# Kernel optimization log

Measured on AMD Instinct MI355X. Metric: run time of the kernel, lower is better.

The kernel has to match this reference:

```python
import jax, jax.numpy as jnp
import numpy as np

PI = 3.1415926  # matches the truncated pi used in the torch source
BS = 8          # DCT block size (qmat.shape[1:] == (8, 8))
NQ = 16         # number of learned quant matrices (qmat.shape[0])
IMG = 64        # nn.Fold output_size=(64, 64)


def dct_matrix(n):
    # Reproduces the (slightly nonstandard) basis built in DCT2d.__init__.
    C = np.zeros((n, n), dtype=np.float32)
    C[0, :] = np.sqrt(1.0 / n)
    for i in range(1, n):
        for j in range(n):
            C[i, j] = np.cos(PI * i * (2 * j + 1) / (2.0 * n)) * np.sqrt(2.0 / n)
    return jnp.asarray(C)


def setup_inputs() -> dict:
    key = jax.random.key(0)
    ks = jax.random.split(key, 9)
    B, Ch = 32, 256
    x = jax.random.normal(ks[0], (B, Ch, IMG, IMG), dtype=jnp.float32)
    noise_level = jax.random.uniform(ks[1], (1,), dtype=jnp.float32)
    # learned parameters
    qmat = jax.random.uniform(ks[2], (NQ, BS, BS), dtype=jnp.float32)
    qmat_weights = jnp.ones((NQ,), dtype=jnp.float32)
    # noise_level_net: Linear(1,16) -> GELU -> Linear(16,16) -> GELU -> Linear(16, 2+NQ)
    w1 = jax.random.normal(ks[3], (1, 16), dtype=jnp.float32) * 0.5
    b1 = jnp.zeros((16,), dtype=jnp.float32)
    w2 = jax.random.normal(ks[4], (16, 16), dtype=jnp.float32) * 0.25
    b2 = jnp.zeros((16,), dtype=jnp.float32)
    w3 = jax.random.normal(ks[5], (16, 2 + NQ), dtype=jnp.float32) * 0.25
    b3 = jnp.zeros((2 + NQ,), dtype=jnp.float32)
    return {"x": x, "noise_level": noise_level, "qmat": qmat,
            "qmat_weights": qmat_weights, "w1": w1, "b1": b1,
            "w2": w2, "b2": b2, "w3": w3, "b3": b3}


def reference(x, noise_level, qmat, qmat_weights, w1, b1, w2, b2, w3, b3):
    B, Ch, H, W = x.shape
    Cm = dct_matrix(BS)
    Cmt = Cm.T

    # noise_level_net (torch.nn.GELU default = exact erf)
    h = jax.nn.gelu(noise_level @ w1 + b1, approximate=False)
    h = jax.nn.gelu(h @ w2 + b2, approximate=False)
    nr = h @ w3 + b3  # [2 + NQ]

    qw = jax.nn.softmax(qmat_weights) * nr[0] + nr[1]          # [NQ]
    learned_qmat = jnp.einsum('i,ihw->hw', qw * nr[2:], qmat)  # [8, 8]

    # unfold into non-overlapping 8x8 blocks: [B*Ch, L, 8, 8], L = (H/8)*(W/8)
    blocks = x.reshape(B * Ch, H // BS, BS, W // BS, BS)
    blocks = blocks.transpose(0, 1, 3, 2, 4).reshape(B * Ch, -1, BS, BS)

    # 2D DCT per block: C @ X @ C^T
    blocks_dct = jnp.einsum('ij,nljk,km->nlim', Cm, blocks, Cmt)
    # IDCT of mask-weighted spectra: C^T @ X @ C
    low = jnp.einsum('ij,nljk,km->nlim', Cmt, blocks_dct * learned_qmat, Cm)
    high = jnp.einsum('ij,nljk,km->nlim', Cmt, blocks_dct * (1.0 - learned_qmat), Cm)

    def fold(b):  # inverse of the unfold above
        b = b.reshape(B * Ch, H // BS, W // BS, BS, BS)
        return b.transpose(0, 1, 3, 2, 4).reshape(B, Ch, H, W)

    return fold(low), fold(high)
```

## Files before the change

### kernel.cpp

```cpp
#include <hip/hip_runtime.h>
#include <math.h>


__host__ __device__ constexpr float cc(int i, int j) {
  constexpr double COS16[32] = {
     1.0,
     0.98078528040323043,
     0.92387953251128674,
     0.83146961230254524,
     0.70710678118654752,
     0.55557023301960222,
     0.38268343236508977,
     0.19509032201612827,
     0.0,
    -0.19509032201612827,
    -0.38268343236508977,
    -0.55557023301960222,
    -0.70710678118654752,
    -0.83146961230254524,
    -0.92387953251128674,
    -0.98078528040323043,
    -1.0,
    -0.98078528040323043,
    -0.92387953251128674,
    -0.83146961230254524,
    -0.70710678118654752,
    -0.55557023301960222,
    -0.38268343236508977,
    -0.19509032201612827,
     0.0,
     0.19509032201612827,
     0.38268343236508977,
     0.55557023301960222,
     0.70710678118654752,
     0.83146961230254524,
     0.92387953251128674,
     0.98078528040323043,
  };
  return (i == 0) ? 0.35355339059327373f
                  : (float)(0.5 * COS16[(i * (2 * j + 1)) % 32]);
}

__global__ void setup_q(const float* __restrict__ noise,
                        const float* __restrict__ qmat,
                        const float* __restrict__ qmw,
                        const float* __restrict__ w1, const float* __restrict__ b1,
                        const float* __restrict__ w2, const float* __restrict__ b2,
                        const float* __restrict__ w3, const float* __restrict__ b3,
                        float* __restrict__ qout) {
  __shared__ double coeff[16];
  if (threadIdx.x == 0) {
    const double inv_sqrt2 = 0.70710678118654752;
    double h1[16], h2[16], nr[18];
    double nl = (double)noise[0];
    for (int j = 0; j < 16; ++j) {
      double v = nl * (double)w1[j] + (double)b1[j];
      h1[j] = 0.5 * v * (1.0 + erf(v * inv_sqrt2));
    }
    for (int j = 0; j < 16; ++j) {
      double v = (double)b2[j];
      for (int i = 0; i < 16; ++i) v += h1[i] * (double)w2[i * 16 + j];
      h2[j] = 0.5 * v * (1.0 + erf(v * inv_sqrt2));
    }
    for (int j = 0; j < 18; ++j) {
      double v = (double)b3[j];
      for (int i = 0; i < 16; ++i) v += h2[i] * (double)w3[i * 18 + j];
      nr[j] = v;
    }
    double mx = (double)qmw[0];
    for (int i = 1; i < 16; ++i) mx = fmax(mx, (double)qmw[i]);
    double e[16], s = 0.0;
    for (int i = 0; i < 16; ++i) { e[i] = exp((double)qmw[i] - mx); s += e[i]; }
    for (int i = 0; i < 16; ++i)
      coeff[i] = (e[i] / s * nr[0] + nr[1]) * nr[2 + i];
  }
  __syncthreads();
  const int t = threadIdx.x;
  double q = 0.0;
  for (int i = 0; i < 16; ++i) q += coeff[i] * (double)qmat[i * 64 + t];
  qout[t] = (float)q;
}

__global__ __launch_bounds__(256) void dct_main(const float* __restrict__ x,
                                                const float* __restrict__ qb,
                                                float* __restrict__ lo,
                                                float* __restrict__ hi) {
  const int gid = blockIdx.x * 256 + threadIdx.x;
  const int base = ((gid >> 6) << 12) | (((gid >> 3) & 7) << 9) | ((gid & 7) << 3);
  const float* px = x + base;

  float X[8][8];
#pragma unroll
  for (int r = 0; r < 8; ++r) {
    const float4 a = *reinterpret_cast<const float4*>(px + r * 64);
    const float4 b = *reinterpret_cast<const float4*>(px + r * 64 + 4);
    X[r][0] = a.x; X[r][1] = a.y; X[r][2] = a.z; X[r][3] = a.w;
    X[r][4] = b.x; X[r][5] = b.y; X[r][6] = b.z; X[r][7] = b.w;
  }

  float U[8][8];
#pragma unroll
  for (int r = 0; r < 8; ++r) {
#pragma unroll
    for (int j = 0; j < 8; ++j) {
      float s = X[r][0] * cc(j, 0);
#pragma unroll
      for (int l = 1; l < 8; ++l) s = fmaf(X[r][l], cc(j, l), s);
      U[r][j] = s;
    }
  }
#pragma unroll
  for (int j = 0; j < 8; ++j) {
    float t[8];
#pragma unroll
    for (int i = 0; i < 8; ++i) {
      float s = cc(i, 0) * U[0][j];
#pragma unroll
      for (int k = 1; k < 8; ++k) s = fmaf(cc(i, k), U[k][j], s);
      t[i] = s;
    }
#pragma unroll
    for (int i = 0; i < 8; ++i) U[i][j] = t[i] * qb[i * 8 + j];
  }
#pragma unroll
  for (int r = 0; r < 8; ++r) {
    float t[8];
#pragma unroll
    for (int j = 0; j < 8; ++j) {
      float s = U[r][0] * cc(0, j);
#pragma unroll
      for (int k = 1; k < 8; ++k) s = fmaf(U[r][k], cc(k, j), s);
      t[j] = s;
    }
#pragma unroll
    for (int j = 0; j < 8; ++j) U[r][j] = t[j];
  }
#pragma unroll
  for (int j = 0; j < 8; ++j) {
    float t[8];
#pragma unroll
    for (int i = 0; i < 8; ++i) {
      float s = cc(0, i) * U[0][j];
#pragma unroll
      for (int k = 1; k < 8; ++k) s = fmaf(cc(k, i), U[k][j], s);
      t[i] = s;
    }
#pragma unroll
    for (int i = 0; i < 8; ++i) U[i][j] = t[i];
  }

  float* plo = lo + base;
  float* phi = hi + base;
#pragma unroll
  for (int r = 0; r < 8; ++r) {
    float4 a = make_float4(U[r][0], U[r][1], U[r][2], U[r][3]);
    float4 b = make_float4(U[r][4], U[r][5], U[r][6], U[r][7]);
    *reinterpret_cast<float4*>(plo + r * 64)     = a;
    *reinterpret_cast<float4*>(plo + r * 64 + 4) = b;
    float4 c = make_float4(X[r][0] - U[r][0], X[r][1] - U[r][1],
                           X[r][2] - U[r][2], X[r][3] - U[r][3]);
    float4 d = make_float4(X[r][4] - U[r][4], X[r][5] - U[r][5],
                           X[r][6] - U[r][6], X[r][7] - U[r][7]);
    *reinterpret_cast<float4*>(phi + r * 64)     = c;
    *reinterpret_cast<float4*>(phi + r * 64 + 4) = d;
  }
}

extern "C" void kernel_launch(void* const* d_in, const int* in_sizes, int n_in,
                              void* d_out, int out_size, void* d_ws, size_t ws_size,
                              hipStream_t stream) {
  const float* x   = (const float*)d_in[0];
  const float* nl  = (const float*)d_in[1];
  const float* qm  = (const float*)d_in[2];
  const float* qmw = (const float*)d_in[3];
  const float* w1  = (const float*)d_in[4];
  const float* b1  = (const float*)d_in[5];
  const float* w2  = (const float*)d_in[6];
  const float* b2  = (const float*)d_in[7];
  const float* w3  = (const float*)d_in[8];
  const float* b3  = (const float*)d_in[9];

  const int n_elem = in_sizes[0];
  float* lo = (float*)d_out;
  float* hi = lo + n_elem;
  float* q  = (float*)d_ws;

  setup_q<<<1, 64, 0, stream>>>(nl, qm, qmw, w1, b1, w2, b2, w3, b3, q);

  const int n_blocks8 = n_elem >> 6;
  const int grid = n_blocks8 >> 8;
  dct_main<<<grid, 256, 0, stream>>>(x, q, lo, hi);
}
```

Before: 466.1 us.

## Fuse quant-matrix setup into DCT kernel and use nontemporal loads/stores

Removes the separate single-block setup kernel and recomputes the small MLP, softmax and 8x8 quant matrix redundantly in every workgroup into shared memory, in float instead of double. Global loads and stores of the streaming image data become nontemporal. This saves one launch and the dependency gap between kernels, at the cost of redundant per-block prologue work, several barriers, and slightly different float precision. Nontemporal hints are meant to reduce cache pollution for the 268 MB-class streaming traffic.

```diff
diff --git a/kernel.cpp b/kernel.cpp
--- a/kernel.cpp
+++ b/kernel.cpp
@@ -1,6 +1,8 @@
 #include <hip/hip_runtime.h>
 #include <math.h>
 
+
+typedef float f4 __attribute__((ext_vector_type(4)));
 
 __host__ __device__ constexpr float cc(int i, int j) {
   constexpr double COS16[32] = {
@@ -41,59 +43,72 @@
                   : (float)(0.5 * COS16[(i * (2 * j + 1)) % 32]);
 }
 
-__global__ void setup_q(const float* __restrict__ noise,
-                        const float* __restrict__ qmat,
-                        const float* __restrict__ qmw,
-                        const float* __restrict__ w1, const float* __restrict__ b1,
-                        const float* __restrict__ w2, const float* __restrict__ b2,
-                        const float* __restrict__ w3, const float* __restrict__ b3,
-                        float* __restrict__ qout) {
-  __shared__ double coeff[16];
-  if (threadIdx.x == 0) {
-    const double inv_sqrt2 = 0.70710678118654752;
-    double h1[16], h2[16], nr[18];
-    double nl = (double)noise[0];
-    for (int j = 0; j < 16; ++j) {
-      double v = nl * (double)w1[j] + (double)b1[j];
-      h1[j] = 0.5 * v * (1.0 + erf(v * inv_sqrt2));
-    }
-    for (int j = 0; j < 16; ++j) {
-      double v = (double)b2[j];
-      for (int i = 0; i < 16; ++i) v += h1[i] * (double)w2[i * 16 + j];
-      h2[j] = 0.5 * v * (1.0 + erf(v * inv_sqrt2));
-    }
-    for (int j = 0; j < 18; ++j) {
-      double v = (double)b3[j];
-      for (int i = 0; i < 16; ++i) v += h2[i] * (double)w3[i * 18 + j];
-      nr[j] = v;
-    }
-    double mx = (double)qmw[0];
-    for (int i = 1; i < 16; ++i) mx = fmax(mx, (double)qmw[i]);
-    double e[16], s = 0.0;
-    for (int i = 0; i < 16; ++i) { e[i] = exp((double)qmw[i] - mx); s += e[i]; }
-    for (int i = 0; i < 16; ++i)
-      coeff[i] = (e[i] / s * nr[0] + nr[1]) * nr[2 + i];
-  }
-  __syncthreads();
-  const int t = threadIdx.x;
-  double q = 0.0;
-  for (int i = 0; i < 16; ++i) q += coeff[i] * (double)qmat[i * 64 + t];
-  qout[t] = (float)q;
-}
-
-__global__ __launch_bounds__(256) void dct_main(const float* __restrict__ x,
-                                                const float* __restrict__ qb,
-                                                float* __restrict__ lo,
-                                                float* __restrict__ hi) {
-  const int gid = blockIdx.x * 256 + threadIdx.x;
+__device__ __forceinline__ float gelu_exact(float v) {
+  return 0.5f * v * (1.0f + erff(v * 0.70710678118654752f));
+}
+
+__global__ __launch_bounds__(256) void dct_fused(
+    const float* __restrict__ x,
+    const float* __restrict__ noise,
+    const float* __restrict__ qmat,
+    const float* __restrict__ qmw,
+    const float* __restrict__ w1, const float* __restrict__ b1,
+    const float* __restrict__ w2, const float* __restrict__ b2,
+    const float* __restrict__ w3, const float* __restrict__ b3,
+    float* __restrict__ lo, float* __restrict__ hi) {
+  __shared__ float Qs[64];
+  __shared__ float s_h1[16], s_h2[16], s_nr[18], s_c[16], s_qw[16];
+
+  const int tid = threadIdx.x;
+
+  if (tid < 16) {
+    float v = noise[0] * w1[tid] + b1[tid];
+    s_h1[tid] = gelu_exact(v);
+    s_qw[tid] = qmw[tid];
+  }
+  __syncthreads();
+  if (tid < 16) {
+    float v = b2[tid];
+#pragma unroll
+    for (int i = 0; i < 16; ++i) v = fmaf(s_h1[i], w2[i * 16 + tid], v);
+    s_h2[tid] = gelu_exact(v);
+  }
+  __syncthreads();
+  if (tid < 18) {
+    float v = b3[tid];
+#pragma unroll
+    for (int i = 0; i < 16; ++i) v = fmaf(s_h2[i], w3[i * 18 + tid], v);
+    s_nr[tid] = v;
+  }
+  __syncthreads();
+  if (tid < 16) {
+    float mx = s_qw[0];
+#pragma unroll
+    for (int i = 1; i < 16; ++i) mx = fmaxf(mx, s_qw[i]);
+    float s = 0.0f;
+#pragma unroll
+    for (int i = 0; i < 16; ++i) s += expf(s_qw[i] - mx);
+    float e = expf(s_qw[tid] - mx);
+    s_c[tid] = (e / s * s_nr[0] + s_nr[1]) * s_nr[2 + tid];
+  }
+  __syncthreads();
+  if (tid < 64) {
+    float q = 0.0f;
+#pragma unroll
+    for (int i = 0; i < 16; ++i) q = fmaf(s_c[i], qmat[i * 64 + tid], q);
+    Qs[tid] = q;
+  }
+  __syncthreads();
+
+  const int gid = blockIdx.x * 256 + tid;
   const int base = ((gid >> 6) << 12) | (((gid >> 3) & 7) << 9) | ((gid & 7) << 3);
   const float* px = x + base;
 
   float X[8][8];
 #pragma unroll
   for (int r = 0; r < 8; ++r) {
-    const float4 a = *reinterpret_cast<const float4*>(px + r * 64);
-    const float4 b = *reinterpret_cast<const float4*>(px + r * 64 + 4);
+    const f4 a = __builtin_nontemporal_load(reinterpret_cast<const f4*>(px + r * 64));
+    const f4 b = __builtin_nontemporal_load(reinterpret_cast<const f4*>(px + r * 64 + 4));
     X[r][0] = a.x; X[r][1] = a.y; X[r][2] = a.z; X[r][3] = a.w;
     X[r][4] = b.x; X[r][5] = b.y; X[r][6] = b.z; X[r][7] = b.w;
   }
@@ -120,7 +135,7 @@
       t[i] = s;
     }
 #pragma unroll
-    for (int i = 0; i < 8; ++i) U[i][j] = t[i] * qb[i * 8 + j];
+    for (int i = 0; i < 8; ++i) U[i][j] = t[i] * Qs[i * 8 + j];
   }
 #pragma unroll
   for (int r = 0; r < 8; ++r) {
@@ -153,16 +168,16 @@
   float* phi = hi + base;
 #pragma unroll
   for (int r = 0; r < 8; ++r) {
-    float4 a = make_float4(U[r][0], U[r][1], U[r][2], U[r][3]);
-    float4 b = make_float4(U[r][4], U[r][5], U[r][6], U[r][7]);
-    *reinterpret_cast<float4*>(plo + r * 64)     = a;
-    *reinterpret_cast<float4*>(plo + r * 64 + 4) = b;
-    float4 c = make_float4(X[r][0] - U[r][0], X[r][1] - U[r][1],
-                           X[r][2] - U[r][2], X[r][3] - U[r][3]);
-    float4 d = make_float4(X[r][4] - U[r][4], X[r][5] - U[r][5],
-                           X[r][6] - U[r][6], X[r][7] - U[r][7]);
-    *reinterpret_cast<float4*>(phi + r * 64)     = c;
-    *reinterpret_cast<float4*>(phi + r * 64 + 4) = d;
+    f4 a = {U[r][0], U[r][1], U[r][2], U[r][3]};
+    f4 b = {U[r][4], U[r][5], U[r][6], U[r][7]};
+    __builtin_nontemporal_store(a, reinterpret_cast<f4*>(plo + r * 64));
+    __builtin_nontemporal_store(b, reinterpret_cast<f4*>(plo + r * 64 + 4));
+    f4 c = {X[r][0] - U[r][0], X[r][1] - U[r][1],
+            X[r][2] - U[r][2], X[r][3] - U[r][3]};
+    f4 d = {X[r][4] - U[r][4], X[r][5] - U[r][5],
+            X[r][6] - U[r][6], X[r][7] - U[r][7]};
+    __builtin_nontemporal_store(c, reinterpret_cast<f4*>(phi + r * 64));
+    __builtin_nontemporal_store(d, reinterpret_cast<f4*>(phi + r * 64 + 4));
   }
 }
 
@@ -183,11 +198,9 @@
   const int n_elem = in_sizes[0];
   float* lo = (float*)d_out;
   float* hi = lo + n_elem;
-  float* q  = (float*)d_ws;
-
-  setup_q<<<1, 64, 0, stream>>>(nl, qm, qmw, w1, b1, w2, b2, w3, b3, q);
 
   const int n_blocks8 = n_elem >> 6;
   const int grid = n_blocks8 >> 8;
-  dct_main<<<grid, 256, 0, stream>>>(x, q, lo, hi);
-}
+  dct_fused<<<grid, 256, 0, stream>>>(x, nl, qm, qmw, w1, b1, w2, b2, w3, b3,
+                                      lo, hi);
+}
```

After: 448.1 us. 3.9% less time.
